# Kernel optimization log

Hardware: AMD Instinct MI355X
Metric: run time of the kernel (lower is better)

## Reference

```python
import jax, jax.numpy as jnp
import numpy as np

B, C, H, W = 4, 256, 48, 48
NH = 4                 # num_heads
HD = C // NH           # head_dim = 64
KD = HD // 2           # key_dim = 32 (attn_ratio=0.5)
QKV_C = C + 2 * KD * NH  # 512
FF = 2 * C             # 512
EPS = 1e-3             # ultralytics BatchNorm2d eps


def _bn(x, g, b, m, v):
    # eval-mode BatchNorm2d over channel dim 1 of NCHW
    s = g / jnp.sqrt(v + EPS)
    return x * s[:, None, None] + (b - m * s)[:, None, None]


def _conv1x1(x, w):
    # w: [out_c, in_c]
    return jnp.einsum('bchw,oc->bohw', x, w)


def _dwconv3x3(x, w):
    # depthwise 3x3, padding 1; w: [C, 1, 3, 3]
    return jax.lax.conv_general_dilated(
        x, w, (1, 1), [(1, 1), (1, 1)],
        dimension_numbers=('NCHW', 'OIHW', 'NCHW'),
        feature_group_count=C)


def setup_inputs() -> dict:
    key = jax.random.key(0)
    ks = jax.random.split(key, 32)
    d = {}
    d['x'] = jax.random.normal(ks[0], (B, C, H, W), dtype=jnp.float32)

    def bn_params(i, ch):
        g = 0.5 + jax.random.uniform(ks[i], (ch,), dtype=jnp.float32)
        b = 0.1 * jax.random.normal(ks[i + 1], (ch,), dtype=jnp.float32)
        m = 0.1 * jax.random.normal(ks[i + 2], (ch,), dtype=jnp.float32)
        v = 0.5 + jax.random.uniform(ks[i + 3], (ch,), dtype=jnp.float32)
        return g, b, m, v

    d['qkv_w'] = 0.05 * jax.random.normal(ks[1], (QKV_C, C), dtype=jnp.float32)
    d['qkv_g'], d['qkv_b'], d['qkv_m'], d['qkv_v'] = bn_params(2, QKV_C)
    d['pe_w'] = 0.1 * jax.random.normal(ks[6], (C, 1, 3, 3), dtype=jnp.float32)
    d['pe_g'], d['pe_b'], d['pe_m'], d['pe_v'] = bn_params(7, C)
    d['proj_w'] = 0.05 * jax.random.normal(ks[11], (C, C), dtype=jnp.float32)
    d['proj_g'], d['proj_b'], d['proj_m'], d['proj_v'] = bn_params(12, C)
    d['f1_w'] = 0.05 * jax.random.normal(ks[16], (FF, C), dtype=jnp.float32)
    d['f1_g'], d['f1_b'], d['f1_m'], d['f1_v'] = bn_params(17, FF)
    d['f2_w'] = 0.05 * jax.random.normal(ks[21], (C, FF), dtype=jnp.float32)
    d['f2_g'], d['f2_b'], d['f2_m'], d['f2_v'] = bn_params(22, C)
    return d


def reference(x, qkv_w, qkv_g, qkv_b, qkv_m, qkv_v,
              pe_w, pe_g, pe_b, pe_m, pe_v,
              proj_w, proj_g, proj_b, proj_m, proj_v,
              f1_w, f1_g, f1_b, f1_m, f1_v,
              f2_w, f2_g, f2_b, f2_m, f2_v):
    b, c, h, w = x.shape
    n = h * w
    # --- Attention ---
    qkv = _bn(_conv1x1(x, qkv_w), qkv_g, qkv_b, qkv_m, qkv_v)
    qkv = qkv.reshape(b, NH, 2 * KD + HD, n)
    q = qkv[:, :, :KD]            # [b, nh, kd, n]
    k = qkv[:, :, KD:2 * KD]      # [b, nh, kd, n]
    v = qkv[:, :, 2 * KD:]        # [b, nh, hd, n]
    attn = jnp.einsum('bhkn,bhkm->bhnm', q, k) * (KD ** -0.5)
    attn = jax.nn.softmax(attn, axis=-1)
    o = jnp.einsum('bhdm,bhnm->bhdn', v, attn).reshape(b, c, h, w)
    pe = _bn(_dwconv3x3(v.reshape(b, c, h, w), pe_w), pe_g, pe_b, pe_m, pe_v)
    attn_out = _bn(_conv1x1(o + pe, proj_w), proj_g, proj_b, proj_m, proj_v)
    x = x + attn_out  # shortcut
    # --- FFN ---
    f = _conv1x1(x, f1_w)
    f = _bn(f, f1_g, f1_b, f1_m, f1_v)
    f = f * jax.nn.sigmoid(f)  # SiLU
    f = _bn(_conv1x1(f, f2_w), f2_g, f2_b, f2_m, f2_v)
    return x + f  # shortcut
```

## Files before the change

### kernel.cpp

```cpp
#include <hip/hip_runtime.h>
#include <math.h>

#define Bb   4
#define Cc   256
#define Hh   48
#define Ww   48
#define NNp  2304
#define Rr   9216
#define NHd  4
#define QKVC 512
#define EPSf 1e-3f

typedef unsigned int   u32;
typedef unsigned short u16;
typedef __attribute__((ext_vector_type(8))) __bf16 bf16x8;
typedef __attribute__((ext_vector_type(4))) float  f32x4;

#if __has_builtin(__builtin_amdgcn_exp2f)
#define EXP2F(x) __builtin_amdgcn_exp2f(x)
#else
#define EXP2F(x) __expf((x) * 0.6931471805599453f)
#endif

__device__ __forceinline__ u16 f2bf(float f) {
    u32 u = __float_as_uint(f);
    u = (u + 0x7fffu + ((u >> 16) & 1u)) >> 16;
    return (u16)u;
}
__device__ __forceinline__ float bf2f(u16 h) {
    return __uint_as_float((u32)h << 16);
}
__device__ __forceinline__ u32 pk2bf(float a, float b) {
    union { __bf16 h; u16 u; } ua, ub;
    ua.h = (__bf16)a; ub.h = (__bf16)b;
    return (u32)ua.u | ((u32)ub.u << 16);
}
__device__ __forceinline__ void gload16(const void* gsrc, void* ldst) {
    __builtin_amdgcn_global_load_lds(
        (const __attribute__((address_space(1))) u32*)gsrc,
        (__attribute__((address_space(3))) u32*)ldst, 16, 0, 0);
}

__global__ __launch_bounds__(256)
void prep_fused(const float* __restrict__ W0, const float* __restrict__ g0, const float* __restrict__ b0, const float* __restrict__ m0, const float* __restrict__ v0, u16* __restrict__ Wb0, float* __restrict__ bi0,
                const float* __restrict__ W1, const float* __restrict__ g1, const float* __restrict__ b1, const float* __restrict__ m1, const float* __restrict__ v1, u16* __restrict__ Wb1, float* __restrict__ bi1,
                const float* __restrict__ W2, const float* __restrict__ g2, const float* __restrict__ b2, const float* __restrict__ m2, const float* __restrict__ v2, u16* __restrict__ Wb2, float* __restrict__ bi2,
                const float* __restrict__ W3, const float* __restrict__ g3, const float* __restrict__ b3, const float* __restrict__ m3, const float* __restrict__ v3, u16* __restrict__ Wb3, float* __restrict__ bi3,
                const float* __restrict__ x, u16* __restrict__ Xt)
{
    const int bid = blockIdx.x;
    const int tid = threadIdx.x;
    if (bid < 384) {
        const int row = bid * 4 + (tid >> 6);
        const int lane = tid & 63;
        const float *W, *gp, *bp, *mp, *vp;
        u16* Wb; float* bias;
        int K = 256, oc;
        float c = 1.f;
        if (row < 512) {
            oc = row; W = W0; gp = g0; bp = b0; mp = m0; vp = v0; Wb = Wb0; bias = bi0;
            if ((oc & 127) < 32) c = 0.17677669529663687f * 1.4426950408889634f;
        } else if (row < 768) {
            oc = row - 512; W = W1; gp = g1; bp = b1; mp = m1; vp = v1; Wb = Wb1; bias = bi1;
        } else if (row < 1280) {
            oc = row - 768; W = W2; gp = g2; bp = b2; mp = m2; vp = v2; Wb = Wb2; bias = bi2;
        } else {
            oc = row - 1280; W = W3; gp = g3; bp = b3; mp = m3; vp = v3; Wb = Wb3; bias = bi3;
            K = 512;
        }
        const float s = gp[oc] * rsqrtf(vp[oc] + EPSf);
        if (lane == 0) bias[oc] = (bp[oc] - mp[oc] * s) * c;
        const float sc = s * c;
        for (int k0 = lane * 4; k0 < K; k0 += 256) {
            const float4 w = *(const float4*)(W + (size_t)oc * K + k0);
            u32 lo = (u32)f2bf(w.x * sc) | ((u32)f2bf(w.y * sc) << 16);
            u32 hi = (u32)f2bf(w.z * sc) | ((u32)f2bf(w.w * sc) << 16);
            *(uint2*)(Wb + (size_t)oc * K + k0) = make_uint2(lo, hi);
        }
        return;
    }
    const int cb = bid - 384;
    const int b  = cb / 144;
    const int rm = cb - b * 144;
    const int c0 = (rm / 36) * 64;
    const int n0 = (rm % 36) * 64;
    __shared__ float tile[64][65];
    {
        const int n = tid & 63, cl = tid >> 6;
        #pragma unroll
        for (int cc = 0; cc < 16; ++cc) {
            const int c = cc * 4 + cl;
            tile[c][n] = x[((size_t)b * Cc + c0 + c) * NNp + n0 + n];
        }
    }
    __syncthreads();
    {
        const int n = tid >> 2, q = tid & 3;
        #pragma unroll
        for (int j = 0; j < 2; ++j) {
            const int ch = q * 2 + j, c = ch * 8;
            u32 w[4];
            #pragma unroll
            for (int e = 0; e < 4; ++e)
                w[e] = (u32)f2bf(tile[c + 2*e][n]) | ((u32)f2bf(tile[c + 2*e + 1][n]) << 16);
            *(uint4*)(Xt + ((size_t)b * NNp + n0 + n) * Cc + c0 + c)
                = make_uint4(w[0], w[1], w[2], w[3]);
        }
    }
}

template<int MODE>
__global__ __launch_bounds__(256)
void gemm64(const u16* __restrict__ A, const u16* __restrict__ Bx,
            const float* __restrict__ bias, const float* __restrict__ resid,
            float* __restrict__ Yf, u16* __restrict__ Yt, int M, int K)
{
    const int r0 = blockIdx.x * 64;
    const int m0 = blockIdx.y * 64;
    const int tid = threadIdx.x;
    const int lane = tid & 63, wid = tid >> 6;
    const int g = lane >> 4, i16 = lane & 15;

    __shared__ __align__(16) u16 Al[2][4][64][8];
    __shared__ __align__(16) u16 Bl[2][4][64][8];

    f32x4 acc[4];
    #pragma unroll
    for (int j = 0; j < 4; ++j) acc[j] = (f32x4){0.f, 0.f, 0.f, 0.f};

    gload16(A + (size_t)(m0 + (tid & 63)) * K + (tid >> 6) * 8,
            (u16*)&Al[0][0][0][0] + (size_t)tid * 8);
    gload16(Bx + (size_t)(r0 + (tid & 63)) * K + (tid >> 6) * 8,
            (u16*)&Bl[0][0][0][0] + (size_t)tid * 8);
    __syncthreads();

    int buf = 0;
    for (int k0 = 0; k0 < K; k0 += 32) {
        if (k0 + 32 < K) {
            const int kn = k0 + 32;
            gload16(A + (size_t)(m0 + (tid & 63)) * K + kn + (tid >> 6) * 8,
                    (u16*)&Al[buf ^ 1][0][0][0] + (size_t)tid * 8);
            gload16(Bx + (size_t)(r0 + (tid & 63)) * K + kn + (tid >> 6) * 8,
                    (u16*)&Bl[buf ^ 1][0][0][0] + (size_t)tid * 8);
        }
        const bf16x8 af = *(const bf16x8*)&Al[buf][g][wid * 16 + i16][0];
        bf16x8 bf[4];
        #pragma unroll
        for (int bo = 0; bo < 4; ++bo)
            bf[bo] = *(const bf16x8*)&Bl[buf][g][bo * 16 + i16][0];
        __builtin_amdgcn_s_setprio(1);
        #pragma unroll
        for (int bo = 0; bo < 4; ++bo)
            acc[bo] = __builtin_amdgcn_mfma_f32_16x16x32_bf16(af, bf[bo], acc[bo], 0, 0, 0);
        __builtin_amdgcn_s_setprio(0);
        __syncthreads();
        buf ^= 1;
    }

    const int b  = r0 / NNp;
    const int nb = r0 - b * NNp;
    const int oc0 = m0 + wid * 16 + g * 4;
    const float4 t4 = *(const float4*)(bias + oc0);
    #pragma unroll
    for (int bo = 0; bo < 4; ++bo) {
        const int nloc = bo * 16 + i16;
        float y[4];
        y[0] = acc[bo][0] + t4.x;  y[1] = acc[bo][1] + t4.y;
        y[2] = acc[bo][2] + t4.z;  y[3] = acc[bo][3] + t4.w;
        if (MODE == 1 || MODE == 3) {
            const int n = nb + nloc;
            const size_t base = ((size_t)b * M + oc0) * NNp + n;
            #pragma unroll
            for (int r = 0; r < 4; ++r) {
                y[r] += resid[base + (size_t)r * NNp];
                Yf[base + (size_t)r * NNp] = y[r];
            }
        }
        if (MODE == 2) {
            #pragma unroll
            for (int r = 0; r < 4; ++r) y[r] = y[r] / (1.f + __expf(-y[r]));
        }
        if (MODE != 3) {
            const size_t rG = (size_t)(r0 + nloc);
            *(uint2*)(Yt + rG * M + oc0) = make_uint2(pk2bf(y[0], y[1]), pk2bf(y[2], y[3]));
        }
    }
}

__global__ __launch_bounds__(256)
void vprep(const u16* __restrict__ Yt, u16* __restrict__ Vb,
           const float* __restrict__ pw,
           const float* __restrict__ gg, const float* __restrict__ bb,
           const float* __restrict__ mm, const float* __restrict__ vv,
           u16* __restrict__ PEb)
{
    const int bid = blockIdx.x;
    const int tid = threadIdx.x;
    if (bid < 576) {
        const int m0 = (bid % 36) * 64;
        const int h  = (bid / 36) & 3;
        const int b  = bid / 144;
        const int bh = b * NHd + h;
        __shared__ u16 vt[64][72];
        #pragma unroll
        for (int ii = 0; ii < 2; ++ii) {
            const int mmr = ii * 32 + (tid >> 3);
            const int ch = tid & 7;
            *(uint4*)&vt[mmr][ch * 8] =
                *(const uint4*)(Yt + ((size_t)b * NNp + m0 + mmr) * QKVC + h * 128 + 64 + ch * 8);
        }
        __syncthreads();
        const int d = tid >> 2, mq = tid & 3;
        #pragma unroll
        for (int j = 0; j < 2; ++j) {
            const int mc = mq * 2 + j;
            u32 w[4];
            #pragma unroll
            for (int e = 0; e < 4; ++e)
                w[e] = (u32)vt[mc * 8 + 2*e][d] | ((u32)vt[mc * 8 + 2*e + 1][d] << 16);
            *(uint4*)(Vb + ((size_t)bh * 64 + d) * NNp + m0 + mc * 8)
                = make_uint4(w[0], w[1], w[2], w[3]);
        }
        return;
    }
    const int pid = bid - 576;
    const int p  = (pid % 72) * 32 + (tid >> 3);
    const int h  = (pid / 72) & 3;
    const int b  = pid / 288;
    const int ch = tid & 7;
    const int c0 = h * 64 + ch * 8;
    const int yy = p / Ww, xx = p - yy * Ww;

    float acc[8];
    #pragma unroll
    for (int j = 0; j < 8; ++j) acc[j] = 0.f;

    #pragma unroll
    for (int dy = -1; dy <= 1; ++dy) {
        const int Y = yy + dy;
        if (Y < 0 || Y >= Hh) continue;
        #pragma unroll
        for (int dx = -1; dx <= 1; ++dx) {
            const int X = xx + dx;
            if (X < 0 || X >= Ww) continue;
            const uint4 raw = *(const uint4*)(Yt +
                ((size_t)b * NNp + Y * Ww + X) * QKVC + h * 128 + 64 + ch * 8);
            const u32* rw = (const u32*)&raw;
            #pragma unroll
            for (int j = 0; j < 8; ++j) {
                const u16 hv = (u16)(rw[j >> 1] >> (16 * (j & 1)));
                acc[j] += pw[(size_t)(c0 + j) * 9 + (dy + 1) * 3 + (dx + 1)] * bf2f(hv);
            }
        }
    }

    u32 res[4];
    #pragma unroll
    for (int e = 0; e < 4; ++e) {
        const int j0 = 2 * e, j1 = 2 * e + 1;
        const float s0 = gg[c0 + j0] * rsqrtf(vv[c0 + j0] + EPSf);
        const float s1 = gg[c0 + j1] * rsqrtf(vv[c0 + j1] + EPSf);
        res[e] = pk2bf(acc[j0] * s0 + (bb[c0 + j0] - mm[c0 + j0] * s0),
                       acc[j1] * s1 + (bb[c0 + j1] - mm[c0 + j1] * s1));
    }
    *(uint4*)(PEb + ((size_t)b * NNp + p) * Cc + c0) = make_uint4(res[0], res[1], res[2], res[3]);
}

__global__ __launch_bounds__(128)
void attn_mfma(const u16* __restrict__ Yt, const u16* __restrict__ Vb,
               u16* __restrict__ PartO, float* __restrict__ Pml)
{
    __shared__ __align__(16) u16 Klds[2][4][64][8];
    __shared__ __align__(16) u16 Vlds[2][64][8][8];
    __shared__ __align__(16) u32 Plds[2][16][36];

    const int tid  = threadIdx.x;
    const int wid  = tid >> 6;
    const int lane = tid & 63;
    const int g    = lane >> 4;
    const int i16  = lane & 15;

    const int wg  = blockIdx.x;
    const int idx = (wg & 7) * 288 + (wg >> 3);
    const int kh  = idx & 1;
    const int qt  = idx >> 1;
    const int xq  = qt % 72;
    const int bh  = qt / 72;
    const int h   = bh & 3, b = bh >> 2;

    const size_t bG = (size_t)b * NNp;
    const u16* Vg = Vb + (size_t)bh * 64 * NNp;

    const int nq = xq * 32 + wid * 16 + i16;
    const bf16x8 qfrag = *(const bf16x8*)(Yt + (bG + nq) * QKVC + h * 128 + g * 8);

    bf16x8 ones;
    { uint4 ov = make_uint4(0x3f803f80u, 0x3f803f80u, 0x3f803f80u, 0x3f803f80u);
      ones = *(bf16x8*)&ov; }

    const f32x4 zero = {0.f, 0.f, 0.f, 0.f};
    f32x4 oacc[4];
    f32x4 lacc = zero;
    #pragma unroll
    for (int d = 0; d < 4; ++d) oacc[d] = zero;
    float m_run = -1e30f;

    const int t0 = kh * 18;

    #pragma unroll
    for (int ii = 0; ii < 2; ++ii) {
        const int ci = ii * 128 + tid;
        gload16(Yt + (bG + t0 * 64 + (ci & 63)) * QKVC + h * 128 + 32 + (ci >> 6) * 8,
                (u16*)&Klds[0][0][0][0] + (size_t)ci * 8);
    }
    #pragma unroll
    for (int ii = 0; ii < 4; ++ii) {
        const int idx2 = ii * 128 + tid;
        const int d = idx2 >> 3, cp = idx2 & 7;
        gload16(Vg + (size_t)d * NNp + t0 * 64 + (cp ^ (d & 7)) * 8,
                (u16*)&Vlds[0][0][0][0] + (size_t)idx2 * 8);
    }
    __syncthreads();

    int cur = 0;
    for (int t = 0; t < 18; ++t) {
        const int m0k = (t0 + t) * 64;
        if (t < 17) {
            const int mn = m0k + 64;
            #pragma unroll
            for (int ii = 0; ii < 2; ++ii) {
                const int ci = ii * 128 + tid;
                gload16(Yt + (bG + mn + (ci & 63)) * QKVC + h * 128 + 32 + (ci >> 6) * 8,
                        (u16*)&Klds[cur ^ 1][0][0][0] + (size_t)ci * 8);
            }
            #pragma unroll
            for (int ii = 0; ii < 4; ++ii) {
                const int idx2 = ii * 128 + tid;
                const int d = idx2 >> 3, cp = idx2 & 7;
                gload16(Vg + (size_t)d * NNp + mn + (cp ^ (d & 7)) * 8,
                        (u16*)&Vlds[cur ^ 1][0][0][0] + (size_t)idx2 * 8);
            }
        }

        f32x4 sac[4];
        __builtin_amdgcn_s_setprio(1);
        #pragma unroll
        for (int j = 0; j < 4; ++j) {
            const bf16x8 kf = *(const bf16x8*)&Klds[cur][g][16 * j + i16][0];
            sac[j] = __builtin_amdgcn_mfma_f32_16x16x32_bf16(kf, qfrag, zero, 0, 0, 0);
        }
        __builtin_amdgcn_s_setprio(0);

        float pm = sac[0][0];
        #pragma unroll
        for (int j = 0; j < 4; ++j)
            #pragma unroll
            for (int r = 0; r < 4; ++r) pm = fmaxf(pm, sac[j][r]);
        pm = fmaxf(pm, __shfl_xor(pm, 16));
        pm = fmaxf(pm, __shfl_xor(pm, 32));

        if (!__all(pm <= m_run + 8.f)) {
            const float mn = fmaxf(m_run, pm);
            const float fc = EXP2F(m_run - mn);
            m_run = mn;
            lacc[0] *= fc; lacc[1] *= fc; lacc[2] *= fc; lacc[3] *= fc;
            #pragma unroll
            for (int d = 0; d < 4; ++d) {
                oacc[d][0] *= fc; oacc[d][1] *= fc;
                oacc[d][2] *= fc; oacc[d][3] *= fc;
            }
        }

        {
            u32* prow = &Plds[wid][i16][0];
            #pragma unroll
            for (int j = 0; j < 4; ++j) {
                const float p0 = EXP2F(sac[j][0] - m_run);
                const float p1 = EXP2F(sac[j][1] - m_run);
                const float p2 = EXP2F(sac[j][2] - m_run);
                const float p3 = EXP2F(sac[j][3] - m_run);
                *(uint2*)&prow[8 * j + 2 * g] = make_uint2(pk2bf(p0, p1), pk2bf(p2, p3));
            }
        }

        const int d7 = i16 & 7;
        __builtin_amdgcn_s_setprio(1);
        #pragma unroll
        for (int s = 0; s < 2; ++s) {
            const bf16x8 pf = *(const bf16x8*)&Plds[wid][i16][16 * s + 4 * g];
            lacc = __builtin_amdgcn_mfma_f32_16x16x32_bf16(ones, pf, lacc, 0, 0, 0);
            #pragma unroll
            for (int db = 0; db < 4; ++db) {
                const bf16x8 vf = *(const bf16x8*)&Vlds[cur][db * 16 + i16][(4 * s + g) ^ d7][0];
                oacc[db] = __builtin_amdgcn_mfma_f32_16x16x32_bf16(vf, pf, oacc[db], 0, 0, 0);
            }
        }
        __builtin_amdgcn_s_setprio(0);

        __syncthreads();
        cur ^= 1;
    }

    const int qloc = wid * 16 + i16;
    const int prow = (qt * 2 + kh) * 32 + qloc;
    if (g == 0) {
        Pml[(size_t)prow * 2 + 0] = m_run;
        Pml[(size_t)prow * 2 + 1] = lacc[0];
    }
    u16* po = PartO + (size_t)prow * 64;
    #pragma unroll
    for (int db = 0; db < 4; ++db) {
        *(uint2*)(po + db * 16 + g * 4) =
            make_uint2(pk2bf(oacc[db][0], oacc[db][1]), pk2bf(oacc[db][2], oacc[db][3]));
    }
}

__global__ __launch_bounds__(256)
void merge_attn(const u16* __restrict__ PartO, const float* __restrict__ Pml,
                u16* __restrict__ Ot)
{
    const int gid = blockIdx.x * 256 + threadIdx.x;
    const int row = gid >> 3;
    const int ch  = gid & 7;
    const int qt  = row >> 5;
    const int q   = row & 31;
    const int bh  = qt / 72;
    const int xq  = qt - bh * 72;
    const int h   = bh & 3, b = bh >> 2;

    const int p0 = (qt * 2) * 32 + q;
    const int p1 = p0 + 32;
    const float2 ml0 = *(const float2*)(Pml + (size_t)p0 * 2);
    const float2 ml1 = *(const float2*)(Pml + (size_t)p1 * 2);
    const float m  = fmaxf(ml0.x, ml1.x);
    const float fa = EXP2F(ml0.x - m);
    const float fb = EXP2F(ml1.x - m);
    const float inv = 1.f / (ml0.y * fa + ml1.y * fb);

    const uint4 a4 = *(const uint4*)(PartO + (size_t)p0 * 64 + ch * 8);
    const uint4 b4 = *(const uint4*)(PartO + (size_t)p1 * 64 + ch * 8);
    u16* dst = Ot + ((size_t)b * NNp + xq * 32 + q) * Cc + h * 64 + ch * 8;
    const uint4 pe4 = *(const uint4*)dst;
    const u32* aw = (const u32*)&a4;
    const u32* bw = (const u32*)&b4;
    const u32* pw = (const u32*)&pe4;
    u32 res[4];
    #pragma unroll
    for (int e = 0; e < 4; ++e) {
        const float y0 = (bf2f((u16)(aw[e] & 0xffff)) * fa + bf2f((u16)(bw[e] & 0xffff)) * fb) * inv
                       + bf2f((u16)(pw[e] & 0xffff));
        const float y1 = (bf2f((u16)(aw[e] >> 16))    * fa + bf2f((u16)(bw[e] >> 16))    * fb) * inv
                       + bf2f((u16)(pw[e] >> 16));
        res[e] = pk2bf(y0, y1);
    }
    *(uint4*)dst = make_uint4(res[0], res[1], res[2], res[3]);
}

extern "C" void kernel_launch(void* const* d_in, const int* in_sizes, int n_in,
                              void* d_out, int out_size, void* d_ws, size_t ws_size,
                              hipStream_t stream)
{
    const float* x      = (const float*)d_in[0];
    const float* qkv_w  = (const float*)d_in[1];
    const float* qkv_g  = (const float*)d_in[2];
    const float* qkv_b  = (const float*)d_in[3];
    const float* qkv_m  = (const float*)d_in[4];
    const float* qkv_v  = (const float*)d_in[5];
    const float* pe_w   = (const float*)d_in[6];
    const float* pe_g   = (const float*)d_in[7];
    const float* pe_b   = (const float*)d_in[8];
    const float* pe_m   = (const float*)d_in[9];
    const float* pe_v   = (const float*)d_in[10];
    const float* proj_w = (const float*)d_in[11];
    const float* proj_g = (const float*)d_in[12];
    const float* proj_b = (const float*)d_in[13];
    const float* proj_m = (const float*)d_in[14];
    const float* proj_v = (const float*)d_in[15];
    const float* f1_w   = (const float*)d_in[16];
    const float* f1_g   = (const float*)d_in[17];
    const float* f1_b   = (const float*)d_in[18];
    const float* f1_m   = (const float*)d_in[19];
    const float* f1_v   = (const float*)d_in[20];
    const float* f2_w   = (const float*)d_in[21];
    const float* f2_g   = (const float*)d_in[22];
    const float* f2_b   = (const float*)d_in[23];
    const float* f2_m   = (const float*)d_in[24];
    const float* f2_v   = (const float*)d_in[25];

    char* wsb = (char*)d_ws;
    u16*   Yt   = (u16*)(wsb);
    u16*   Xt   = (u16*)(wsb + 9437184);
    u16*   Vb   = (u16*)(wsb + 14155776);
    u16*   Ot   = (u16*)(wsb + 18874368);
    float* x1f  = (float*)(wsb + 23592960);
    u16*   Wq   = (u16*)(wsb + 33030144);
    u16*   Wp   = (u16*)(wsb + 33292288);
    u16*   W1   = (u16*)(wsb + 33423360);
    u16*   W2   = (u16*)(wsb + 33685504);
    float* biq  = (float*)(wsb + 33947648);
    float* bip  = (float*)(wsb + 33949696);
    float* bi1  = (float*)(wsb + 33950720);
    float* bi2  = (float*)(wsb + 33952768);
    u16*   Ft   = Yt;
    u16*   X1t  = Xt;
    float* Pml  = (float*)Xt;
    u16*   PartO= (u16*)x1f;
    float* out  = (float*)d_out;

    prep_fused<<<dim3(960), dim3(256), 0, stream>>>(
        qkv_w, qkv_g, qkv_b, qkv_m, qkv_v, Wq, biq,
        proj_w, proj_g, proj_b, proj_m, proj_v, Wp, bip,
        f1_w, f1_g, f1_b, f1_m, f1_v, W1, bi1,
        f2_w, f2_g, f2_b, f2_m, f2_v, W2, bi2,
        x, Xt);

    gemm64<0><<<dim3(144, 8), dim3(256), 0, stream>>>(
        Wq, Xt, biq, nullptr, nullptr, Yt, QKVC, 256);

    vprep<<<dim3(1728), dim3(256), 0, stream>>>(
        Yt, Vb, pe_w, pe_g, pe_b, pe_m, pe_v, Ot);

    attn_mfma<<<dim3(2304), dim3(128), 0, stream>>>(Yt, Vb, PartO, Pml);
    merge_attn<<<dim3(1152), dim3(256), 0, stream>>>(PartO, Pml, Ot);

    gemm64<1><<<dim3(144, 4), dim3(256), 0, stream>>>(
        Wp, Ot, bip, x, x1f, X1t, Cc, 256);

    gemm64<2><<<dim3(144, 8), dim3(256), 0, stream>>>(
        W1, X1t, bi1, nullptr, nullptr, Ft, QKVC, 256);

    gemm64<3><<<dim3(144, 4), dim3(256), 0, stream>>>(
        W2, Ft, bi2, x1f, out, nullptr, Cc, 512);
}
```

Measured before the change: 146.3 us.

## Halve attention key tile to 32 and relayout V shared memory without swizzle

Shrinks the per-iteration key/value tile in the attention kernel from 64 to 32 keys, doubling the loop count to 36. The K, V and P shared buffers shrink to match, and V moves to an MFMA-fragment-ordered layout [db][g][i16][8], which removes the XOR swizzle. This lowers LDS use and register pressure per iteration, which may allow more resident blocks. The cost is twice as many barriers, online-softmax max updates and prefetch issues per key.

After: 158.3 us. +8.2%, slower.

```diff
diff --git a/kernel.cpp b/kernel.cpp
--- a/kernel.cpp
+++ b/kernel.cpp
@@ -270,9 +270,9 @@
 void attn_mfma(const u16* __restrict__ Yt, const u16* __restrict__ Vb,
                u16* __restrict__ PartO, float* __restrict__ Pml)
 {
-    __shared__ __align__(16) u16 Klds[2][4][64][8];
-    __shared__ __align__(16) u16 Vlds[2][64][8][8];
-    __shared__ __align__(16) u32 Plds[2][16][36];
+    __shared__ __align__(16) u16 Klds[2][4][32][8];
+    __shared__ __align__(16) u16 Vlds[2][4][4][16][8];
+    __shared__ __align__(16) u32 Plds[2][16][20];
 
     const int tid  = threadIdx.x;
     const int wid  = tid >> 6;
@@ -305,57 +305,48 @@
     for (int d = 0; d < 4; ++d) oacc[d] = zero;
     float m_run = -1e30f;
 
-    const int t0 = kh * 18;
-
+    const int t0 = kh * 36;
+
+    gload16(Yt + (bG + t0 * 32 + (tid & 31)) * QKVC + h * 128 + 32 + (tid >> 5) * 8,
+            (u16*)&Klds[0][0][0][0] + (size_t)tid * 8);
     #pragma unroll
     for (int ii = 0; ii < 2; ++ii) {
-        const int ci = ii * 128 + tid;
-        gload16(Yt + (bG + t0 * 64 + (ci & 63)) * QKVC + h * 128 + 32 + (ci >> 6) * 8,
-                (u16*)&Klds[0][0][0][0] + (size_t)ci * 8);
-    }
-    #pragma unroll
-    for (int ii = 0; ii < 4; ++ii) {
-        const int idx2 = ii * 128 + tid;
-        const int d = idx2 >> 3, cp = idx2 & 7;
-        gload16(Vg + (size_t)d * NNp + t0 * 64 + (cp ^ (d & 7)) * 8,
-                (u16*)&Vlds[0][0][0][0] + (size_t)idx2 * 8);
+        const int i2 = ii * 128 + tid;
+        const int d  = ((i2 >> 6) << 4) + (i2 & 15);
+        const int c  = (i2 >> 4) & 3;
+        gload16(Vg + (size_t)d * NNp + t0 * 32 + c * 8,
+                (u16*)&Vlds[0][0][0][0][0] + (size_t)i2 * 8);
     }
     __syncthreads();
 
     int cur = 0;
-    for (int t = 0; t < 18; ++t) {
-        const int m0k = (t0 + t) * 64;
-        if (t < 17) {
-            const int mn = m0k + 64;
+    for (int t = 0; t < 36; ++t) {
+        const int m0k = (t0 + t) * 32;
+        if (t < 35) {
+            const int mn = m0k + 32;
+            gload16(Yt + (bG + mn + (tid & 31)) * QKVC + h * 128 + 32 + (tid >> 5) * 8,
+                    (u16*)&Klds[cur ^ 1][0][0][0] + (size_t)tid * 8);
             #pragma unroll
             for (int ii = 0; ii < 2; ++ii) {
-                const int ci = ii * 128 + tid;
-                gload16(Yt + (bG + mn + (ci & 63)) * QKVC + h * 128 + 32 + (ci >> 6) * 8,
-                        (u16*)&Klds[cur ^ 1][0][0][0] + (size_t)ci * 8);
+                const int i2 = ii * 128 + tid;
+                const int d  = ((i2 >> 6) << 4) + (i2 & 15);
+                const int c  = (i2 >> 4) & 3;
+                gload16(Vg + (size_t)d * NNp + mn + c * 8,
+                        (u16*)&Vlds[cur ^ 1][0][0][0][0] + (size_t)i2 * 8);
             }
-            #pragma unroll
-            for (int ii = 0; ii < 4; ++ii) {
-                const int idx2 = ii * 128 + tid;
-                const int d = idx2 >> 3, cp = idx2 & 7;
-                gload16(Vg + (size_t)d * NNp + mn + (cp ^ (d & 7)) * 8,
-                        (u16*)&Vlds[cur ^ 1][0][0][0] + (size_t)idx2 * 8);
-            }
-        }
-
-        f32x4 sac[4];
+        }
+
+        f32x4 sac[2];
         __builtin_amdgcn_s_setprio(1);
         #pragma unroll
-        for (int j = 0; j < 4; ++j) {
+        for (int j = 0; j < 2; ++j) {
             const bf16x8 kf = *(const bf16x8*)&Klds[cur][g][16 * j + i16][0];
             sac[j] = __builtin_amdgcn_mfma_f32_16x16x32_bf16(kf, qfrag, zero, 0, 0, 0);
         }
         __builtin_amdgcn_s_setprio(0);
 
-        float pm = sac[0][0];
-        #pragma unroll
-        for (int j = 0; j < 4; ++j)
-            #pragma unroll
-            for (int r = 0; r < 4; ++r) pm = fmaxf(pm, sac[j][r]);
+        float pm = fmaxf(fmaxf(fmaxf(sac[0][0], sac[0][1]), fmaxf(sac[0][2], sac[0][3])),
+                         fmaxf(fmaxf(sac[1][0], sac[1][1]), fmaxf(sac[1][2], sac[1][3])));
         pm = fmaxf(pm, __shfl_xor(pm, 16));
         pm = fmaxf(pm, __shfl_xor(pm, 32));
 
@@ -374,7 +365,7 @@
         {
             u32* prow = &Plds[wid][i16][0];
             #pragma unroll
-            for (int j = 0; j < 4; ++j) {
+            for (int j = 0; j < 2; ++j) {
                 const float p0 = EXP2F(sac[j][0] - m_run);
                 const float p1 = EXP2F(sac[j][1] - m_run);
                 const float p2 = EXP2F(sac[j][2] - m_run);
@@ -383,15 +374,13 @@
             }
         }
 
-        const int d7 = i16 & 7;
         __builtin_amdgcn_s_setprio(1);
-        #pragma unroll
-        for (int s = 0; s < 2; ++s) {
-            const bf16x8 pf = *(const bf16x8*)&Plds[wid][i16][16 * s + 4 * g];
+        {
+            const bf16x8 pf = *(const bf16x8*)&Plds[wid][i16][4 * g];
             lacc = __builtin_amdgcn_mfma_f32_16x16x32_bf16(ones, pf, lacc, 0, 0, 0);
             #pragma unroll
             for (int db = 0; db < 4; ++db) {
-                const bf16x8 vf = *(const bf16x8*)&Vlds[cur][db * 16 + i16][(4 * s + g) ^ d7][0];
+                const bf16x8 vf = *(const bf16x8*)&Vlds[cur][db][g][i16][0];
                 oacc[db] = __builtin_amdgcn_mfma_f32_16x16x32_bf16(vf, pf, oacc[db], 0, 0, 0);
             }
         }
```
